# Kernel tuning notes

Hardware: AMD Instinct MI355X
Metric: run time of the kernel (lower is better)

## Reference

```python
import jax, jax.numpy as jnp
import numpy as np
from jax.scipy.linalg import solve_triangular

EPS = 1e-5
CHUNK = 64

def _rms(x, w, eps=EPS):
    return x * jax.lax.rsqrt(jnp.mean(x * x, axis=-1, keepdims=True) + eps) * w

def _l2norm(x, eps=1e-6):
    return x * jax.lax.rsqrt(jnp.sum(x * x, axis=-1, keepdims=True) + eps)

def _causal_conv(x, w):
    # x: [B,T,C], w: [C,K] depthwise causal short conv
    K = w.shape[1]
    T = x.shape[1]
    xp = jnp.pad(x, ((0, 0), (K - 1, 0), (0, 0)))
    return sum(xp[:, j:j + T, :] * w[:, j] for j in range(K))

def _chunk_gated_delta_rule(q, k, v, g, beta, chunk=CHUNK):
    # q,k: [B,H,T,Dk] (l2-normalized, q pre-scaled); v: [B,H,T,Dv]; g,beta: [B,H,T]
    Bb, H, T, Dk = k.shape
    Dv = v.shape[-1]
    N = T // chunk
    qc, kc, vc = (a.reshape(Bb, H, N, chunk, -1) for a in (q, k, v))
    gc = g.reshape(Bb, H, N, chunk)
    bc = beta.reshape(Bb, H, N, chunk)
    gcs = jnp.cumsum(gc, axis=-1)  # within-chunk cumulative log-decay
    tri = jnp.tril(jnp.ones((chunk, chunk), bool))
    tri_s = jnp.tril(jnp.ones((chunk, chunk), bool), -1)
    diff = gcs[..., :, None] - gcs[..., None, :]
    decay = jnp.where(tri, jnp.exp(jnp.where(tri, diff, 0.0)), 0.0)  # [B,H,N,C,C]
    k_beta = kc * bc[..., None]
    v_beta = vc * bc[..., None]
    A = jnp.einsum('bhnck,bhndk->bhncd', k_beta, kc) * decay
    A = jnp.where(tri_s, A, 0.0)
    eye = jnp.eye(chunk, dtype=q.dtype)
    Tmat = solve_triangular(eye + A, jnp.broadcast_to(eye, A.shape), lower=True)  # (I+A)^-1
    u = Tmat @ v_beta                               # [B,H,N,C,Dv]
    w = Tmat @ (k_beta * jnp.exp(gcs)[..., None])   # [B,H,N,C,Dk]

    def step(S, inp):
        q_i, k_i, u_i, w_i, g_i, dm_i = inp
        attn = jnp.where(tri, jnp.einsum('bhck,bhdk->bhcd', q_i, k_i) * dm_i, 0.0)
        v_new = u_i - w_i @ S
        o_i = (q_i * jnp.exp(g_i)[..., None]) @ S + attn @ v_new
        g_last = g_i[..., -1]
        k_dec = k_i * jnp.exp(g_last[..., None] - g_i)[..., None]
        S = S * jnp.exp(g_last)[..., None, None] + jnp.einsum('bhck,bhcv->bhkv', k_dec, v_new)
        return S, o_i

    xs = tuple(jnp.moveaxis(a, 2, 0) for a in (qc, kc, u, w, gcs, decay))
    S0 = jnp.zeros((Bb, H, Dk, Dv), q.dtype)
    _, outs = jax.lax.scan(step, S0, xs)  # [N,B,H,C,Dv]
    return jnp.moveaxis(outs, 0, 2).reshape(Bb, H, T, Dv)

def _layer_forward(x, mask, ln1_w, qkvz_w, ba_w, conv_w, A_log, dt_bias,
                   o_norm_w, out_w, ln2_w, gate_w, up_w, down_w):
    B, T, D = x.shape
    H = A_log.shape[0]
    kd = qkvz_w.shape[0] // 4  # key_dim == value_dim here (k_heads==v_heads, Dk==Dv)
    vd = kd
    Dk = kd // H
    Dv = vd // H
    silu = jax.nn.silu
    h = _rms(x, ln1_w)
    qkvz = h @ qkvz_w.T
    q, k, v, z = jnp.split(qkvz, [kd, 2 * kd, 2 * kd + vd], axis=-1)
    b, a = jnp.split(h @ ba_w.T, 2, axis=-1)  # [B,T,H] each
    mixed = jnp.concatenate([q, k, v], axis=-1) * mask[..., None]
    mixed = silu(_causal_conv(mixed, conv_w))
    q, k, v = jnp.split(mixed, [kd, 2 * kd], axis=-1)
    q = _l2norm(q.reshape(B, T, H, Dk))
    k = _l2norm(k.reshape(B, T, H, Dk))
    v = v.reshape(B, T, H, Dv)
    beta = jax.nn.sigmoid(b) * mask[..., None]
    g = -jnp.exp(A_log) * jax.nn.softplus(a + dt_bias) * mask[..., None]
    scale = Dk ** -0.5
    bhtd = lambda t: jnp.transpose(t, (0, 2, 1, 3))
    o = _chunk_gated_delta_rule(bhtd(q) * scale, bhtd(k), bhtd(v),
                                jnp.transpose(g, (0, 2, 1)), jnp.transpose(beta, (0, 2, 1)))
    o = jnp.transpose(o, (0, 2, 1, 3))  # [B,T,H,Dv]
    o = _rms(o, o_norm_w) * silu(z.reshape(B, T, H, Dv))  # gated RMSNorm
    x = x + o.reshape(B, T, vd) @ out_w.T
    h2 = _rms(x, ln2_w)
    mlp_out = (silu(h2 @ gate_w.T) * (h2 @ up_w.T)) @ down_w.T
    return x + mlp_out

def setup_inputs():
    key = jax.random.key(0)
    ks = jax.random.split(key, 12)
    B, T, D, H, Dk, Dv, M, K = 1, 4096, 2048, 16, 128, 128, 8192, 4
    kd, vd = H * Dk, H * Dv
    nrm = lambda i, shp, sc=0.02: jax.random.normal(ks[i], shp, jnp.float32) * sc
    return {
        'x': nrm(0, (B, T, D), 1.0),
        'mask': jnp.ones((B, T), jnp.float32),
        'ln1_w': jnp.ones((D,), jnp.float32),
        'qkvz_w': nrm(1, (2 * kd + 2 * vd, D)),
        'ba_w': nrm(2, (2 * H, D)),
        'conv_w': nrm(3, (2 * kd + vd, K), 0.3),
        'A_log': jnp.log(jax.random.uniform(ks[4], (H,), jnp.float32, 1.0, 16.0)),
        'dt_bias': nrm(5, (H,), 0.5),
        'o_norm_w': jnp.ones((Dv,), jnp.float32),
        'out_w': nrm(6, (D, vd)),
        'ln2_w': jnp.ones((D,), jnp.float32),
        'gate_w': nrm(7, (M, D)),
        'up_w': nrm(8, (M, D)),
        'down_w': nrm(9, (D, M)),
    }

def reference(x, mask, ln1_w, qkvz_w, ba_w, conv_w, A_log, dt_bias,
              o_norm_w, out_w, ln2_w, gate_w, up_w, down_w):
    return _layer_forward(x, mask, ln1_w, qkvz_w, ba_w, conv_w, A_log, dt_bias,
                          o_norm_w, out_w, ln2_w, gate_w, up_w, down_w)
```

## Files before the change

kernel.cpp:

```cpp
#include <hip/hip_runtime.h>
#include <math.h>

#define T_LEN 4096
#define DMODEL 2048
#define NH 16
#define CQKV 6144
#define CQKVZ 8192
#define SCALE 0.08838834764831845f

using bf16x8 = __attribute__((ext_vector_type(8))) short;
using f32x4  = __attribute__((ext_vector_type(4))) float;

__device__ __forceinline__ float siluf(float x) { return x / (1.0f + __expf(-x)); }

__device__ __forceinline__ unsigned short f2bf(float f) {
  unsigned int u = __float_as_uint(f);
  u = (u + 0x7FFFu + ((u >> 16) & 1u)) >> 16;
  return (unsigned short)u;
}
__device__ __forceinline__ float bf2f(unsigned short u) {
  return __uint_as_float(((unsigned int)u) << 16);
}
__device__ __forceinline__ ushort4 pack4(float a, float b, float c, float d) {
  ushort4 r; r.x = f2bf(a); r.y = f2bf(b); r.z = f2bf(c); r.w = f2bf(d); return r;
}

__device__ __forceinline__ void gl_lds16(const unsigned short* g, unsigned short* l) {
  __builtin_amdgcn_global_load_lds(
      (const __attribute__((address_space(1))) void*)g,
      (__attribute__((address_space(3))) void*)l, 16, 0, 0);
}

template<int MODE>
__global__ __launch_bounds__(256) void rmsnorm_kernel(const float* __restrict__ x,
                                                      const float* __restrict__ w,
                                                      float* __restrict__ outf,
                                                      unsigned short* __restrict__ outb) {
  const int t = blockIdx.x;
  const int tid = threadIdx.x;
  const float4* xr = (const float4*)(x + (size_t)t * DMODEL);
  float4 v0 = xr[tid];
  float4 v1 = xr[tid + 256];
  float s = v0.x*v0.x + v0.y*v0.y + v0.z*v0.z + v0.w*v0.w
          + v1.x*v1.x + v1.y*v1.y + v1.z*v1.z + v1.w*v1.w;
#pragma unroll
  for (int off = 32; off > 0; off >>= 1) s += __shfl_down(s, off);
  __shared__ float red[4];
  if ((tid & 63) == 0) red[tid >> 6] = s;
  __syncthreads();
  const float tot = red[0] + red[1] + red[2] + red[3];
  const float r = rsqrtf(tot * (1.0f / DMODEL) + 1e-5f);
  const float4* wr = (const float4*)w;
  const float4 w0 = wr[tid], w1 = wr[tid + 256];
  float4 o0, o1;
  o0.x = v0.x*r*w0.x; o0.y = v0.y*r*w0.y; o0.z = v0.z*r*w0.z; o0.w = v0.w*r*w0.w;
  o1.x = v1.x*r*w1.x; o1.y = v1.y*r*w1.y; o1.z = v1.z*r*w1.z; o1.w = v1.w*r*w1.w;
  if (MODE == 1) {
    float4* orow = (float4*)(outf + (size_t)t * DMODEL);
    orow[tid] = o0;
    orow[tid + 256] = o1;
  }
  ushort4* brow = (ushort4*)(outb + (size_t)t * DMODEL);
  brow[tid] = pack4(o0.x, o0.y, o0.z, o0.w);
  brow[tid + 256] = pack4(o1.x, o1.y, o1.z, o1.w);
}

__global__ __launch_bounds__(256) void f2b_kernel(const float* __restrict__ in,
                                                  unsigned short* __restrict__ out) {
  const size_t i = (size_t)blockIdx.x * 256 + threadIdx.x;
  const float4 a = ((const float4*)in)[2 * i];
  const float4 b = ((const float4*)in)[2 * i + 1];
  ((ushort4*)out)[2 * i] = pack4(a.x, a.y, a.z, a.w);
  ((ushort4*)out)[2 * i + 1] = pack4(b.x, b.y, b.z, b.w);
}

template<int EPI, int BM>
__global__ __launch_bounds__(512, 1) void gemm256_kernel(const unsigned short* __restrict__ A,
                                                         const unsigned short* __restrict__ B,
                                                         float* __restrict__ Cf,
                                                         unsigned short* __restrict__ Cb,
                                                         int M, int N, int K) {
  constexpr int BN = 256;
  constexpr int MI = BM / 32;
  constexpr int AW = BM / 128;
  __shared__ __align__(16) unsigned short lds[3][(BM + BN) * 32];
  const int nbm = M / BM, nbn = N / BN, nwg = nbm * nbn;
  const int nt = K >> 5;
  int bmi, bni;
  {
    const int bid = blockIdx.x;
    const int cpx = nwg >> 3;
    int sc = 1;
    while (sc * sc < cpx) sc <<= 1;
    if (sc * sc > cpx) sc >>= 1;
    const int scn = (sc > 0) ? (cpx / sc) : 0;
    if ((nwg & 7) == 0 && sc > 0 && sc * scn == cpx && (nbm % sc) == 0 && (nbn % scn) == 0) {
      const int chunk = bid & 7, widx = bid >> 3;
      const int regc = nbn / scn;
      bmi = (chunk / regc) * sc + widx / scn;
      bni = (chunk % regc) * scn + widx % scn;
    } else {
      bmi = bid / nbn; bni = bid % nbn;
    }
  }
  const int bm = bmi * BM, bn = bni * BN;
  const int tid = threadIdx.x;
  const int wv = tid >> 6, ln = tid & 63;
  const int fr = ln & 15, qq = ln >> 4;
  const int wm = wv >> 2, wn = wv & 3;
  const int ra0 = wm * (BM / 2), rb0 = wn * 64;
  const int lrow = ln >> 2;
  const int lslot = ln & 3;

  f32x4 acc[MI][4];
  const f32x4 zero = {0.f, 0.f, 0.f, 0.f};
#pragma unroll
  for (int mi = 0; mi < MI; mi++)
#pragma unroll
    for (int ni = 0; ni < 4; ni++) acc[mi][ni] = zero;

  auto stageA = [&](int buf, int t) {
    const int k0 = t << 5;
#pragma unroll
    for (int q = 0; q < AW; q++) {
      const int lr = q * 128 + wv * 16 + lrow;
      const int sl = lslot ^ ((lr >> 1) & 3);
      gl_lds16(A + (size_t)(bm + lr) * K + k0 + sl * 8,
               &lds[buf][(q * 128 + wv * 16) * 32]);
    }
  };
  auto stageB = [&](int buf, int t) {
    const int k0 = t << 5;
#pragma unroll
    for (int q = 0; q < 2; q++) {
      const int lr = q * 128 + wv * 16 + lrow;
      const int sl = lslot ^ ((lr >> 1) & 3);
      gl_lds16(B + (size_t)(bn + lr) * K + k0 + sl * 8,
               &lds[buf][BM * 32 + (q * 128 + wv * 16) * 32]);
    }
  };

  stageA(0, 0); stageB(0, 0);
  stageA(1, 1); stageB(1, 1);
  if constexpr (AW == 2) asm volatile("s_waitcnt vmcnt(4)" ::: "memory");
  else                   asm volatile("s_waitcnt vmcnt(3)" ::: "memory");
  __builtin_amdgcn_s_barrier();
  asm volatile("" ::: "memory");

  for (int t = 0; t < nt; t++) {
    const int cb = t % 3;
    const int b2 = (t + 2) % 3;
    const unsigned short* lA = &lds[cb][0];
    const unsigned short* lB = &lds[cb][BM * 32];
    bf16x8 bfr[4];
#pragma unroll
    for (int ni = 0; ni < 4; ni++) {
      const int r = rb0 + ni * 16 + fr;
      bfr[ni] = *(const bf16x8*)&lB[r * 32 + ((qq ^ ((r >> 1) & 3)) << 3)];
    }
    bf16x8 afr[MI];
#pragma unroll
    for (int mi = 0; mi < MI; mi++) {
      const int r = ra0 + mi * 16 + fr;
      afr[mi] = *(const bf16x8*)&lA[r * 32 + ((qq ^ ((r >> 1) & 3)) << 3)];
    }
    if (t + 2 < nt) { stageA(b2, t + 2); stageB(b2, t + 2); }
    __builtin_amdgcn_s_setprio(1);
#pragma unroll
    for (int mi = 0; mi < MI; mi++)
#pragma unroll
      for (int ni = 0; ni < 4; ni++)
        acc[mi][ni] = __builtin_amdgcn_mfma_f32_16x16x32_bf16(afr[mi], bfr[ni], acc[mi][ni], 0, 0, 0);
    __builtin_amdgcn_s_setprio(0);
    if (t + 1 < nt) {
      asm volatile("s_waitcnt lgkmcnt(0)" ::: "memory");
      if (t + 2 < nt) {
        if constexpr (AW == 2) asm volatile("s_waitcnt vmcnt(4)" ::: "memory");
        else                   asm volatile("s_waitcnt vmcnt(3)" ::: "memory");
      } else {
        asm volatile("s_waitcnt vmcnt(0)" ::: "memory");
      }
      __builtin_amdgcn_s_barrier();
      asm volatile("" ::: "memory");
    }
  }

  const int cm4 = qq * 4;
#pragma unroll
  for (int mi = 0; mi < MI; mi++) {
#pragma unroll
    for (int ni = 0; ni < 4; ni++) {
#pragma unroll
      for (int r = 0; r < 4; r++) {
        const int grow = bm + ra0 + mi * 16 + cm4 + r;
        const int gcol = bn + rb0 + ni * 16 + fr;
        const size_t off = (size_t)grow * N + gcol;
        const float v = acc[mi][ni][r];
        if (EPI == 0) {
          Cb[off] = f2bf(v);
        } else if (EPI == 1) {
          Cf[off] += v;
        } else {
          Cb[off] = f2bf(siluf(bf2f(Cb[off])) * v);
        }
      }
    }
  }
}

__global__ __launch_bounds__(256) void ba_gemm_kernel(const float* __restrict__ h_in,
                                                      const float* __restrict__ ba_w,
                                                      float* __restrict__ ba_out) {
  __shared__ __align__(16) float hl[2048];
  __shared__ float red[32][9];
  const int t = blockIdx.x;
  const int tid = threadIdx.x;
  const float4* hr = (const float4*)(h_in + (size_t)t * DMODEL);
  ((float4*)hl)[tid] = hr[tid];
  ((float4*)hl)[tid + 256] = hr[tid + 256];
  __syncthreads();
  const int c = tid & 31;
  const int p = tid >> 5;
  const float* wrow = ba_w + (size_t)c * DMODEL + p * 256;
  const float* hrow = hl + p * 256;
  float s = 0.f;
#pragma unroll 8
  for (int k = 0; k < 256; k++) s += hrow[k] * wrow[k];
  red[c][p] = s;
  __syncthreads();
  if (tid < 32) {
    float tot = 0.f;
#pragma unroll
    for (int q = 0; q < 8; q++) tot += red[tid][q];
    ba_out[(size_t)t * 32 + tid] = tot;
  }
}

__global__ __launch_bounds__(256) void zcopy_kernel(const unsigned short* __restrict__ qkvz,
                                                    unsigned short* __restrict__ z) {
  const int idx = blockIdx.x * 256 + threadIdx.x;
  const int t = idx >> 8;
  const int c8 = (idx & 255) * 8;
  *(uint4*)(z + (size_t)t * 2048 + c8) =
      *(const uint4*)(qkvz + (size_t)t * CQKVZ + CQKV + c8);
}

__global__ __launch_bounds__(256) void conv_silu_kernel(const unsigned short* __restrict__ qkvz,
                                                        const float* __restrict__ conv_w,
                                                        const float* __restrict__ mask,
                                                        float* __restrict__ mixed) {
  const int idx = blockIdx.x * 256 + threadIdx.x;
  const int c4 = (idx % 1536) * 4;
  const int t = idx / 1536;
  const float4 w0 = *(const float4*)(conv_w + (size_t)c4 * 4);
  const float4 w1 = *(const float4*)(conv_w + (size_t)c4 * 4 + 4);
  const float4 w2 = *(const float4*)(conv_w + (size_t)c4 * 4 + 8);
  const float4 w3 = *(const float4*)(conv_w + (size_t)c4 * 4 + 12);
  const float wj0[4] = {w0.x, w0.y, w0.z, w0.w};
  const float wj1[4] = {w1.x, w1.y, w1.z, w1.w};
  const float wj2[4] = {w2.x, w2.y, w2.z, w2.w};
  const float wj3[4] = {w3.x, w3.y, w3.z, w3.w};
  float4 acc = make_float4(0.f, 0.f, 0.f, 0.f);
#pragma unroll
  for (int j = 0; j < 4; j++) {
    const int tt = t - 3 + j;
    if (tt < 0) continue;
    const float m = mask[tt];
    const ushort4 xb = *(const ushort4*)(qkvz + (size_t)tt * CQKVZ + c4);
    acc.x += bf2f(xb.x) * m * wj0[j];
    acc.y += bf2f(xb.y) * m * wj1[j];
    acc.z += bf2f(xb.z) * m * wj2[j];
    acc.w += bf2f(xb.w) * m * wj3[j];
  }
  acc.x = siluf(acc.x); acc.y = siluf(acc.y); acc.z = siluf(acc.z); acc.w = siluf(acc.w);
  *(float4*)(mixed + (size_t)t * CQKV + c4) = acc;
}

__global__ __launch_bounds__(256) void l2norm_kernel(float* __restrict__ mixed) {
  const int r = blockIdx.x * 4 + (threadIdx.x >> 6);
  const int lane = threadIdx.x & 63;
  const int t = r >> 5;
  const int hh = r & 31;
  float* p = mixed + (size_t)t * CQKV + hh * 128 + lane * 2;
  float2 v = *(float2*)p;
  float s = v.x * v.x + v.y * v.y;
#pragma unroll
  for (int off = 32; off > 0; off >>= 1) s += __shfl_down(s, off);
  s = __shfl(s, 0);
  const float rn = rsqrtf(s + 1e-6f);
  v.x *= rn; v.y *= rn;
  *(float2*)p = v;
}

__global__ __launch_bounds__(256) void beta_g_kernel(const float* __restrict__ ba,
                                                     const float* __restrict__ A_log,
                                                     const float* __restrict__ dt_bias,
                                                     const float* __restrict__ mask,
                                                     float* __restrict__ beta,
                                                     float* __restrict__ g) {
  const int idx = blockIdx.x * 256 + threadIdx.x;
  const int t = idx >> 4;
  const int h = idx & 15;
  const float b = ba[(size_t)t * 32 + h];
  const float a = ba[(size_t)t * 32 + 16 + h];
  const float m = mask[t];
  beta[idx] = m / (1.0f + expf(-b));
  const float xx = a + dt_bias[h];
  const float sp = (xx > 20.0f) ? xx : log1pf(expf(xx));
  g[idx] = -expf(A_log[h]) * sp * m;
}

__global__ __launch_bounds__(256) void gcs_kernel(const float* __restrict__ g,
                                                  float* __restrict__ gcsbuf,
                                                  float* __restrict__ edkbuf,
                                                  float* __restrict__ egqbuf,
                                                  float* __restrict__ adecbuf) {
  const int idx = blockIdx.x * 256 + threadIdx.x;
  if (idx >= 1024) return;
  const int h = idx >> 6;
  const int n = idx & 63;
  const int t0 = n * 64;
  float s = 0.f;
  for (int i = 0; i < 64; i++) {
    s += g[(size_t)(t0 + i) * NH + h];
    gcsbuf[(size_t)idx * 64 + i] = s;
  }
  const float glast = s;
  adecbuf[idx] = __expf(glast);
  for (int i = 0; i < 64; i++) {
    const float gi = gcsbuf[(size_t)idx * 64 + i];
    edkbuf[(size_t)idx * 64 + i] = __expf(glast - gi);
    egqbuf[(size_t)idx * 64 + i] = __expf(gi) * SCALE;
  }
}

__global__ __launch_bounds__(256) void pre_attn_kernel(const float* __restrict__ mixed,
                                                       const float* __restrict__ gcsbuf,
                                                       const float* __restrict__ betabuf,
                                                       float* __restrict__ abuf,
                                                       float* __restrict__ attnbuf) {
  __shared__ __align__(16) float kl[64][132];
  __shared__ float gcs_s[64];
  __shared__ float betal[64];
  const int blk = blockIdx.x;
  const int h = blk >> 6;
  const int n = blk & 63;
  const int t0 = n * 64;
  const int tid = threadIdx.x;
  if (tid < 64) {
    gcs_s[tid] = gcsbuf[(size_t)blk * 64 + tid];
    betal[tid] = betabuf[(size_t)(t0 + tid) * NH + h];
  }
#pragma unroll
  for (int rep = 0; rep < 8; rep++) {
    const int lin = rep * 256 + tid;
    const int i = lin >> 5;
    const int d = (lin & 31) * 4;
    const float4 kv = *(const float4*)(mixed + (size_t)(t0 + i) * CQKV + 2048 + h * 128 + d);
    *(float4*)&kl[i][d] = kv;
  }
  __syncthreads();
  const int cj = tid & 15;
  const int ri = tid >> 4;
  const int i0 = ri * 4, j0 = cj * 4;
  float accA[4][4], accQ[4][4];
#pragma unroll
  for (int a = 0; a < 4; a++)
#pragma unroll
    for (int b = 0; b < 4; b++) { accA[a][b] = 0.f; accQ[a][b] = 0.f; }
  const float* qbase = mixed + (size_t)t0 * CQKV + h * 128;
#pragma unroll 4
  for (int d = 0; d < 128; d++) {
    const float kj0 = kl[j0][d], kj1 = kl[j0 + 1][d], kj2 = kl[j0 + 2][d], kj3 = kl[j0 + 3][d];
#pragma unroll
    for (int a = 0; a < 4; a++) {
      const float ka = kl[i0 + a][d];
      const float qa = qbase[(size_t)(i0 + a) * CQKV + d];
      accA[a][0] += ka * kj0; accA[a][1] += ka * kj1; accA[a][2] += ka * kj2; accA[a][3] += ka * kj3;
      accQ[a][0] += qa * kj0; accQ[a][1] += qa * kj1; accQ[a][2] += qa * kj2; accQ[a][3] += qa * kj3;
    }
  }
#pragma unroll
  for (int a = 0; a < 4; a++) {
    const int i = i0 + a;
    const float gi = gcs_s[i];
    const float bi = betal[i];
    float4 Av, Qv;
    float dec;
    dec = __expf(fminf(gi - gcs_s[j0 + 0], 0.f));
    Av.x = (i > j0 + 0) ? accA[a][0] * bi * dec : 0.f;
    Qv.x = (i >= j0 + 0) ? accQ[a][0] * dec * SCALE : 0.f;
    dec = __expf(fminf(gi - gcs_s[j0 + 1], 0.f));
    Av.y = (i > j0 + 1) ? accA[a][1] * bi * dec : 0.f;
    Qv.y = (i >= j0 + 1) ? accQ[a][1] * dec * SCALE : 0.f;
    dec = __expf(fminf(gi - gcs_s[j0 + 2], 0.f));
    Av.z = (i > j0 + 2) ? accA[a][2] * bi * dec : 0.f;
    Qv.z = (i >= j0 + 2) ? accQ[a][2] * dec * SCALE : 0.f;
    dec = __expf(fminf(gi - gcs_s[j0 + 3], 0.f));
    Av.w = (i > j0 + 3) ? accA[a][3] * bi * dec : 0.f;
    Qv.w = (i >= j0 + 3) ? accQ[a][3] * dec * SCALE : 0.f;
    *(float4*)(abuf + (size_t)blk * 4096 + i * 64 + j0) = Av;
    *(float4*)(attnbuf + (size_t)blk * 4096 + i * 64 + j0) = Qv;
  }
}

__global__ __launch_bounds__(256) void pre_solve_kernel(const float* __restrict__ abuf,
                                                        const float* __restrict__ betabuf,
                                                        float* __restrict__ tbuf) {
  __shared__ float Al[64][65];
  __shared__ float Tl[64][65];
  const int blk = blockIdx.x;
  const int h = blk >> 6;
  const int n = blk & 63;
  const int t0 = n * 64;
  const int tid = threadIdx.x;
#pragma unroll
  for (int rep = 0; rep < 4; rep++) {
    const int lin = rep * 256 + tid;
    const int i = lin >> 4;
    const int j = (lin & 15) * 4;
    const float4 av = *(const float4*)(abuf + (size_t)blk * 4096 + i * 64 + j);
    Al[i][j] = av.x; Al[i][j + 1] = av.y; Al[i][j + 2] = av.z; Al[i][j + 3] = av.w;
  }
  __syncthreads();
  if (tid < 64) {
    const int j = tid;
    const float bj = betabuf[(size_t)(t0 + j) * NH + h];
    for (int i = 0; i < 64; i++) {
      float s = (i == j) ? 1.0f : 0.0f;
      for (int l = j; l < i; l++) s -= Al[i][l] * Tl[l][j];
      Tl[i][j] = s;
    }
    for (int i = j; i < 64; i++) Tl[i][j] *= bj;
  }
  __syncthreads();
#pragma unroll
  for (int rep = 0; rep < 4; rep++) {
    const int lin = rep * 256 + tid;
    const int i = lin >> 4;
    const int j = (lin & 15) * 4;
    float4 tv;
    tv.x = Tl[i][j]; tv.y = Tl[i][j + 1]; tv.z = Tl[i][j + 2]; tv.w = Tl[i][j + 3];
    *(float4*)(tbuf + (size_t)blk * 4096 + i * 64 + j) = tv;
  }
}

__global__ __launch_bounds__(256) void pre_uw_kernel(const float* __restrict__ mixed,
                                                     const float* __restrict__ tbuf,
                                                     const float* __restrict__ gcsbuf,
                                                     float* __restrict__ ubuf,
                                                     unsigned short* __restrict__ wbf) {
  __shared__ __align__(16) float Tl[64][68];
  __shared__ __align__(16) float xl[64][132];
  __shared__ float egcs[64];
  const int blk = blockIdx.x;
  const int h = blk >> 6;
  const int n = blk & 63;
  const int t0 = n * 64;
  const int tid = threadIdx.x;
  if (tid < 64) egcs[tid] = __expf(gcsbuf[(size_t)blk * 64 + tid]);
#pragma unroll
  for (int rep = 0; rep < 4; rep++) {
    const int lin = rep * 256 + tid;
    const int i = lin >> 4;
    const int j = (lin & 15) * 4;
    const float4 tv = *(const float4*)(tbuf + (size_t)blk * 4096 + i * 64 + j);
    *(float4*)&Tl[i][j] = tv;
  }
#pragma unroll
  for (int rep = 0; rep < 8; rep++) {
    const int lin = rep * 256 + tid;
    const int i = lin >> 5;
    const int d = (lin & 31) * 4;
    const float4 vv = *(const float4*)(mixed + (size_t)(t0 + i) * CQKV + 4096 + h * 128 + d);
    *(float4*)&xl[i][d] = vv;
  }
  __syncthreads();
  const int cgu = tid & 15;
  const int riu = tid >> 4;
  const int i0 = riu * 4;
  const int d0 = cgu * 8;
  float acc[4][8];
#pragma unroll
  for (int a = 0; a < 4; a++)
#pragma unroll
    for (int b = 0; b < 8; b++) acc[a][b] = 0.f;
#pragma unroll 2
  for (int j = 0; j < 64; j++) {
    const float tv[4] = {Tl[i0][j], Tl[i0 + 1][j], Tl[i0 + 2][j], Tl[i0 + 3][j]};
    const float4 x0 = *(const float4*)&xl[j][d0];
    const float4 x1 = *(const float4*)&xl[j][d0 + 4];
    const float xv[8] = {x0.x, x0.y, x0.z, x0.w, x1.x, x1.y, x1.z, x1.w};
#pragma unroll
    for (int a = 0; a < 4; a++)
#pragma unroll
      for (int b = 0; b < 8; b++) acc[a][b] += tv[a] * xv[b];
  }
#pragma unroll
  for (int a = 0; a < 4; a++) {
    float* up = ubuf + (size_t)(t0 + i0 + a) * 2048 + h * 128 + d0;
    *(float4*)up = make_float4(acc[a][0], acc[a][1], acc[a][2], acc[a][3]);
    *(float4*)(up + 4) = make_float4(acc[a][4], acc[a][5], acc[a][6], acc[a][7]);
  }
  __syncthreads();
#pragma unroll
  for (int rep = 0; rep < 8; rep++) {
    const int lin = rep * 256 + tid;
    const int i = lin >> 5;
    const int d = (lin & 31) * 4;
    float4 kv = *(const float4*)(mixed + (size_t)(t0 + i) * CQKV + 2048 + h * 128 + d);
    const float e = egcs[i];
    kv.x *= e; kv.y *= e; kv.z *= e; kv.w *= e;
    *(float4*)&xl[i][d] = kv;
  }
  __syncthreads();
#pragma unroll
  for (int a = 0; a < 4; a++)
#pragma unroll
    for (int b = 0; b < 8; b++) acc[a][b] = 0.f;
#pragma unroll 2
  for (int j = 0; j < 64; j++) {
    const float tv[4] = {Tl[i0][j], Tl[i0 + 1][j], Tl[i0 + 2][j], Tl[i0 + 3][j]};
    const float4 x0 = *(const float4*)&xl[j][d0];
    const float4 x1 = *(const float4*)&xl[j][d0 + 4];
    const float xv[8] = {x0.x, x0.y, x0.z, x0.w, x1.x, x1.y, x1.z, x1.w};
#pragma unroll
    for (int a = 0; a < 4; a++)
#pragma unroll
      for (int b = 0; b < 8; b++) acc[a][b] += tv[a] * xv[b];
  }
#pragma unroll
  for (int a = 0; a < 4; a++) {
    const int l = i0 + a;
    unsigned short* wp = wbf + (size_t)(t0 + l) * 2048 + h * 128 + ((cgu ^ (l & 7)) << 3);
    *(ushort4*)wp = pack4(-acc[a][0], -acc[a][1], -acc[a][2], -acc[a][3]);
    *(ushort4*)(wp + 4) = pack4(-acc[a][4], -acc[a][5], -acc[a][6], -acc[a][7]);
  }
}

__global__ __launch_bounds__(256) void ktrans_kernel(const float* __restrict__ mixed,
                                                     const float* __restrict__ edkbuf,
                                                     const float* __restrict__ egqbuf,
                                                     unsigned short* __restrict__ kdT,
                                                     unsigned short* __restrict__ qe) {
  __shared__ __align__(16) float kl[64][132];
  __shared__ float edk_s[64];
  __shared__ float egq_s[64];
  const int blk = blockIdx.x;
  const int h = blk >> 6;
  const int n = blk & 63;
  const int t0 = n * 64;
  const int tid = threadIdx.x;
  if (tid < 64) {
    edk_s[tid] = edkbuf[(size_t)blk * 64 + tid];
    egq_s[tid] = egqbuf[(size_t)blk * 64 + tid];
  }
#pragma unroll
  for (int q = 0; q < 8; q++) {
    const int idx = tid + q * 256;
    const int l = idx >> 5, c4 = (idx & 31) * 4;
    *(float4*)&kl[l][c4] = *(const float4*)(mixed + (size_t)(t0 + l) * CQKV + 2048 + h * 128 + c4);
  }
  __syncthreads();
#pragma unroll
  for (int q = 0; q < 4; q++) {
    const int idx = tid + q * 256;
    const int d = idx >> 3, lsl = idx & 7;
    const int l8 = lsl * 8;
    float v[8];
#pragma unroll
    for (int j = 0; j < 8; j++) v[j] = kl[l8 + j][d] * edk_s[l8 + j];
    unsigned short* p = kdT + (size_t)blk * 8192 + d * 64 + ((lsl ^ (d & 7)) << 3);
    *(ushort4*)p = pack4(v[0], v[1], v[2], v[3]);
    *(ushort4*)(p + 4) = pack4(v[4], v[5], v[6], v[7]);
  }
#pragma unroll
  for (int q = 0; q < 8; q++) {
    const int idx = tid + q * 256;
    const int i = idx >> 5, c4 = (idx & 31) * 4;
    const float4 v = *(const float4*)(mixed + (size_t)(t0 + i) * CQKV + h * 128 + c4);
    const float e = egq_s[i];
    *(ushort4*)(qe + (size_t)(t0 + i) * 2048 + h * 128 + c4) =
        pack4(v.x * e, v.y * e, v.z * e, v.w * e);
  }
}

__global__ __launch_bounds__(512, 1) void scan_kernel(const unsigned short* __restrict__ wbf,
                                                      const unsigned short* __restrict__ kdT,
                                                      const float* __restrict__ ubuf,
                                                      const float* __restrict__ adecbuf,
                                                      unsigned short* __restrict__ STb,
                                                      unsigned short* __restrict__ vtb,
                                                      const float* __restrict__ gw,
                                                      const float* __restrict__ uw,
                                                      const float* __restrict__ dw,
                                                      const float* __restrict__ ow,
                                                      const float* __restrict__ xin,
                                                      unsigned short* __restrict__ Wg,
                                                      unsigned short* __restrict__ Wu,
                                                      unsigned short* __restrict__ Wd,
                                                      unsigned short* __restrict__ Wo,
                                                      float* __restrict__ outc) {
  __shared__ __align__(16) unsigned short stage[2][16384];
  __shared__ __align__(16) unsigned short privAll[8][3072];
  if (blockIdx.x >= 16) {
    const int xb = blockIdx.x - 16;
    const int tid = threadIdx.x;
    if (xb < 13312) {
      const float* src; unsigned short* dst; size_t u;
      if (xb < 4096)       { src = gw; dst = Wg; u = (size_t)xb * 512 + tid; }
      else if (xb < 8192)  { src = uw; dst = Wu; u = (size_t)(xb - 4096) * 512 + tid; }
      else if (xb < 12288) { src = dw; dst = Wd; u = (size_t)(xb - 8192) * 512 + tid; }
      else                 { src = ow; dst = Wo; u = (size_t)(xb - 12288) * 512 + tid; }
      const float4 a = ((const float4*)src)[2 * u];
      const float4 b = ((const float4*)src)[2 * u + 1];
      ((ushort4*)dst)[2 * u] = pack4(a.x, a.y, a.z, a.w);
      ((ushort4*)dst)[2 * u + 1] = pack4(b.x, b.y, b.z, b.w);
    } else {
      const size_t i = (size_t)(xb - 13312) * 512 + tid;
      ((float4*)outc)[2 * i] = ((const float4*)xin)[2 * i];
      ((float4*)outc)[2 * i + 1] = ((const float4*)xin)[2 * i + 1];
    }
    return;
  }
  const int h = blockIdx.x;
  const int tid = threadIdx.x;
  const int ln = tid & 63;
  const int wv = tid >> 6;
  const int fr = ln & 15;
  const int g  = ln >> 4;
  const int c0 = wv * 16;
  const int fsw = fr & 7;
  unsigned short* privA = &privAll[wv][0];
  unsigned short* privB = &privAll[wv][2048];
  const f32x4 zero = {0.f, 0.f, 0.f, 0.f};

  f32x4 acc2[8];
#pragma unroll
  for (int dt = 0; dt < 8; dt++) acc2[dt] = zero;

  auto stage_wk = [&](int buf, int n1) {
    const int t0n = n1 * 64;
    const size_t kbase = (size_t)(h * 64 + n1) * 8192;
#pragma unroll
    for (int q = 0; q < 2; q++) {
      const int m = wv * 2 + q;
      gl_lds16(wbf + (size_t)(t0n + m * 4 + (ln >> 4)) * 2048 + h * 128 + (ln & 15) * 8,
               &stage[buf][m * 512]);
      gl_lds16(kdT + kbase + (m * 8 + (ln >> 3)) * 64 + (ln & 7) * 8,
               &stage[buf][8192 + m * 512]);
    }
  };

  float ur[4][4];
#pragma unroll
  for (int lt = 0; lt < 4; lt++)
#pragma unroll
    for (int r = 0; r < 4; r++)
      ur[lt][r] = ubuf[(size_t)(lt * 16 + g * 4 + r) * 2048 + h * 128 + c0 + fr];
  float ad = adecbuf[h * 64];
  stage_wk(0, 0);
  asm volatile("s_waitcnt vmcnt(0)" ::: "memory");
  __builtin_amdgcn_s_barrier();
  asm volatile("" ::: "memory");

  for (int n = 0; n < 64; n++) {
    const int blk = h * 64 + n;
    const unsigned short* wl = &stage[n & 1][0];
    const unsigned short* kl = &stage[n & 1][8192];
    if (n + 1 < 64) stage_wk((n + 1) & 1, n + 1);
    __builtin_amdgcn_sched_barrier(0);
    float urn[4][4];
    float adn = 0.f;
    if (n + 1 < 64) {
      const int t1 = (n + 1) * 64;
#pragma unroll
      for (int lt = 0; lt < 4; lt++)
#pragma unroll
        for (int r = 0; r < 4; r++)
          urn[lt][r] = ubuf[(size_t)(t1 + lt * 16 + g * 4 + r) * 2048 + h * 128 + c0 + fr];
      adn = adecbuf[blk + 1];
    } else {
#pragma unroll
      for (int lt = 0; lt < 4; lt++)
#pragma unroll
        for (int r = 0; r < 4; r++) urn[lt][r] = 0.f;
    }
    __builtin_amdgcn_sched_barrier(0);
#pragma unroll
    for (int dt = 0; dt < 8; dt++) {
      const int slot = dt * 2 + (g >> 1);
      const ushort4 pv = pack4(acc2[dt][0], acc2[dt][1], acc2[dt][2], acc2[dt][3]);
      *(ushort4*)&privA[fr * 128 + ((slot ^ fsw) << 3) + (g & 1) * 4] = pv;
      *(ushort4*)(STb + (size_t)blk * 16384 + (c0 + fr) * 128 + dt * 16 + g * 4) = pv;
    }
    f32x4 acc1[4];
#pragma unroll
    for (int lt = 0; lt < 4; lt++) {
      f32x4 t;
      t[0] = ur[lt][0]; t[1] = ur[lt][1]; t[2] = ur[lt][2]; t[3] = ur[lt][3];
      acc1[lt] = t;
    }
#pragma unroll
    for (int ks = 0; ks < 4; ks++) {
      const int kb = ks * 4 + g;
      const bf16x8 b = *(const bf16x8*)&privA[fr * 128 + ((kb ^ fsw) << 3)];
#pragma unroll
      for (int lt = 0; lt < 4; lt++) {
        const bf16x8 a = *(const bf16x8*)&wl[(lt * 16 + fr) * 128 + ((kb ^ fsw) << 3)];
        acc1[lt] = __builtin_amdgcn_mfma_f32_16x16x32_bf16(a, b, acc1[lt], 0, 0, 0);
      }
    }
#pragma unroll
    for (int lt = 0; lt < 4; lt++) {
      const int slot = lt * 2 + (g >> 1);
      const ushort4 pv = pack4(acc1[lt][0], acc1[lt][1], acc1[lt][2], acc1[lt][3]);
      *(ushort4*)&privB[fr * 64 + ((slot ^ fsw) << 3) + (g & 1) * 4] = pv;
      *(ushort4*)(vtb + (size_t)blk * 8192 + (c0 + fr) * 64 + lt * 16 + g * 4) = pv;
    }
#pragma unroll
    for (int dt = 0; dt < 8; dt++) {
      acc2[dt][0] *= ad; acc2[dt][1] *= ad; acc2[dt][2] *= ad; acc2[dt][3] *= ad;
    }
#pragma unroll
    for (int ks = 0; ks < 2; ks++) {
      const int kb = ks * 4 + g;
      const bf16x8 b = *(const bf16x8*)&privB[fr * 64 + ((kb ^ fsw) << 3)];
#pragma unroll
      for (int dt = 0; dt < 8; dt++) {
        const bf16x8 a = *(const bf16x8*)&kl[(dt * 16 + fr) * 64 + ((kb ^ fsw) << 3)];
        acc2[dt] = __builtin_amdgcn_mfma_f32_16x16x32_bf16(a, b, acc2[dt], 0, 0, 0);
      }
    }
#pragma unroll
    for (int lt = 0; lt < 4; lt++)
#pragma unroll
      for (int r = 0; r < 4; r++) ur[lt][r] = urn[lt][r];
    ad = adn;
    if (n + 1 < 64) {
      asm volatile("s_waitcnt lgkmcnt(0)" ::: "memory");
      __builtin_amdgcn_sched_barrier(0);
      asm volatile("s_waitcnt vmcnt(29)" ::: "memory");
      __builtin_amdgcn_sched_barrier(0);
      __builtin_amdgcn_s_barrier();
      __builtin_amdgcn_sched_barrier(0);
    }
  }
}

__global__ __launch_bounds__(256) void ocomp_kernel(const unsigned short* __restrict__ qe,
                                                    const unsigned short* __restrict__ STbuf,
                                                    const unsigned short* __restrict__ vtbuf,
                                                    const float* __restrict__ attnbuf,
                                                    const unsigned short* __restrict__ zb,
                                                    const float* __restrict__ onw,
                                                    unsigned short* __restrict__ ob) {
  __shared__ __align__(16) unsigned short STl[128 * 128];
  __shared__ __align__(16) unsigned short vtl[128 * 64];
  __shared__ __align__(16) unsigned short ql[64 * 128];
  __shared__ __align__(16) unsigned short al[64 * 64];
  const int blk = blockIdx.x;
  const int h = blk >> 6;
  const int n = blk & 63;
  const int t0 = n * 64;
  const int tid = threadIdx.x;
#pragma unroll
  for (int q = 0; q < 8; q++) {
    const int idx = tid + q * 256;
    const int c = idx >> 4, dg = idx & 15;
    *(uint4*)&STl[c * 128 + ((dg ^ (c & 7)) << 3)] =
        *(const uint4*)(STbuf + (size_t)blk * 16384 + c * 128 + dg * 8);
  }
#pragma unroll
  for (int q = 0; q < 4; q++) {
    const int idx = tid + q * 256;
    const int c = idx >> 3, lg = idx & 7;
    *(uint4*)&vtl[c * 64 + ((lg ^ (c & 7)) << 3)] =
        *(const uint4*)(vtbuf + (size_t)blk * 8192 + c * 64 + lg * 8);
  }
#pragma unroll
  for (int q = 0; q < 4; q++) {
    const int idx = tid + q * 256;
    const int i = idx >> 4, dg = idx & 15;
    *(uint4*)&ql[i * 128 + ((dg ^ (i & 7)) << 3)] =
        *(const uint4*)(qe + (size_t)(t0 + i) * 2048 + h * 128 + dg * 8);
  }
#pragma unroll
  for (int q = 0; q < 4; q++) {
    const int idx = tid + q * 256;
    const int i = idx >> 4, l4 = (idx & 15) * 4;
    const float4 v = *(const float4*)(attnbuf + (size_t)blk * 4096 + i * 64 + l4);
    *(ushort4*)&al[i * 64 + (((l4 >> 3) ^ (i & 7)) << 3) + (l4 & 7)] =
        pack4(v.x, v.y, v.z, v.w);
  }
  __syncthreads();
  const int ln = tid & 63;
  const int wv = tid >> 6;
  const int fr = ln & 15;
  const int g = ln >> 4;
  const int i0 = wv * 16;
  f32x4 acc[8];
  const f32x4 zero = {0.f, 0.f, 0.f, 0.f};
#pragma unroll
  for (int nt = 0; nt < 8; nt++) acc[nt] = zero;
#pragma unroll
  for (int ks = 0; ks < 4; ks++) {
    const int kb = ks * 4 + g;
    const int ar = i0 + fr;
    const bf16x8 a = *(const bf16x8*)&ql[ar * 128 + ((kb ^ (ar & 7)) << 3)];
#pragma unroll
    for (int nt = 0; nt < 8; nt++) {
      const int c = nt * 16 + fr;
      const bf16x8 b = *(const bf16x8*)&STl[c * 128 + ((kb ^ (c & 7)) << 3)];
      acc[nt] = __builtin_amdgcn_mfma_f32_16x16x32_bf16(a, b, acc[nt], 0, 0, 0);
    }
  }
#pragma unroll
  for (int ks = 0; ks < 2; ks++) {
    const int kb = ks * 4 + g;
    const int ar = i0 + fr;
    const bf16x8 a = *(const bf16x8*)&al[ar * 64 + ((kb ^ (ar & 7)) << 3)];
#pragma unroll
    for (int nt = 0; nt < 8; nt++) {
      const int c = nt * 16 + fr;
      const bf16x8 b = *(const bf16x8*)&vtl[c * 64 + ((kb ^ (c & 7)) << 3)];
      acc[nt] = __builtin_amdgcn_mfma_f32_16x16x32_bf16(a, b, acc[nt], 0, 0, 0);
    }
  }
  float s0 = 0.f, s1 = 0.f, s2 = 0.f, s3 = 0.f;
#pragma unroll
  for (int nt = 0; nt < 8; nt++) {
    s0 += acc[nt][0] * acc[nt][0];
    s1 += acc[nt][1] * acc[nt][1];
    s2 += acc[nt][2] * acc[nt][2];
    s3 += acc[nt][3] * acc[nt][3];
  }
#pragma unroll
  for (int m = 1; m < 16; m <<= 1) {
    s0 += __shfl_xor(s0, m);
    s1 += __shfl_xor(s1, m);
    s2 += __shfl_xor(s2, m);
    s3 += __shfl_xor(s3, m);
  }
  float rn[4];
  rn[0] = rsqrtf(s0 * (1.0f / 128.0f) + 1e-5f);
  rn[1] = rsqrtf(s1 * (1.0f / 128.0f) + 1e-5f);
  rn[2] = rsqrtf(s2 * (1.0f / 128.0f) + 1e-5f);
  rn[3] = rsqrtf(s3 * (1.0f / 128.0f) + 1e-5f);
#pragma unroll
  for (int nt = 0; nt < 8; nt++) {
    const int c = nt * 16 + fr;
    const float wn = onw[c];
#pragma unroll
    for (int r = 0; r < 4; r++) {
      const size_t off = (size_t)(t0 + i0 + g * 4 + r) * 2048 + h * 128 + c;
      const float zz = siluf(bf2f(zb[off]));
      ob[off] = f2bf(acc[nt][r] * rn[r] * wn * zz);
    }
  }
}

extern "C" void kernel_launch(void* const* d_in, const int* in_sizes, int n_in,
                              void* d_out, int out_size, void* d_ws, size_t ws_size,
                              hipStream_t stream) {
  (void)in_sizes; (void)n_in; (void)out_size;
  const float* x        = (const float*)d_in[0];
  const float* mask     = (const float*)d_in[1];
  const float* ln1_w    = (const float*)d_in[2];
  const float* qkvz_w   = (const float*)d_in[3];
  const float* ba_w     = (const float*)d_in[4];
  const float* conv_w   = (const float*)d_in[5];
  const float* A_log    = (const float*)d_in[6];
  const float* dt_bias  = (const float*)d_in[7];
  const float* o_norm_w = (const float*)d_in[8];
  const float* out_w    = (const float*)d_in[9];
  const float* ln2_w    = (const float*)d_in[10];
  const float* gate_w   = (const float*)d_in[11];
  const float* up_w     = (const float*)d_in[12];
  const float* down_w   = (const float*)d_in[13];
  float* out = (float*)d_out;

  const size_t NEED_BYTES = (size_t)75825152 * 4;
  if (ws_size < NEED_BYTES) return;

  float* ws = (float*)d_ws;
  float* mixed_buf = ws;
  unsigned short* Wg = (unsigned short*)ws;
  unsigned short* Wu = (unsigned short*)(ws + 8388608);
  unsigned short* Wd = (unsigned short*)(ws + 16777216);
  unsigned short* qkvz_bf = (unsigned short*)(ws + 25165824);
  float* u_buf = ws + 25165824;
  unsigned short* wbf = (unsigned short*)(ws + 33554432);
  unsigned short* kdT = (unsigned short*)(ws + 37748736);
  unsigned short* gate_bf = (unsigned short*)(ws + 25165824);
  unsigned short* z_bf = (unsigned short*)(ws + 41943040);
  float* h_buf = ws + 46137344;
  float* a_buf = ws + 46137344;
  unsigned short* vt_buf = (unsigned short*)(ws + 46137344);
  float* t_buf = ws + 50331648;
  unsigned short* qe_bf = (unsigned short*)(ws + 50331648);
  unsigned short* h_bf  = (unsigned short*)(ws + 54525952);
  unsigned short* ob    = (unsigned short*)(ws + 54525952);
  unsigned short* h2_bf = (unsigned short*)(ws + 54525952);
  float* attn_buf = ws + 58720256;
  unsigned short* Wq = (unsigned short*)(ws + 62914560);
  unsigned short* ST_buf = (unsigned short*)(ws + 62914560);
  unsigned short* Wo = (unsigned short*)(ws + 71303168);
  float* ba_buf   = ws + 73400320;
  float* beta_buf = ws + 73531392;
  float* g_buf    = ws + 73596928;
  float* gcs_buf  = ws + 73662464;
  float* edk_buf  = ws + 73728000;
  float* egq_buf  = ws + 73793536;
  float* adec_buf = ws + 73859072;

  rmsnorm_kernel<1><<<4096, 256, 0, stream>>>(x, ln1_w, h_buf, h_bf);
  f2b_kernel<<<8192, 256, 0, stream>>>(qkvz_w, Wq);
  gemm256_kernel<0, 256><<<512, 512, 0, stream>>>(h_bf, Wq, nullptr, qkvz_bf, 4096, 8192, 2048);
  ba_gemm_kernel<<<4096, 256, 0, stream>>>(h_buf, ba_w, ba_buf);
  zcopy_kernel<<<4096, 256, 0, stream>>>(qkvz_bf, z_bf);
  conv_silu_kernel<<<24576, 256, 0, stream>>>(qkvz_bf, conv_w, mask, mixed_buf);
  l2norm_kernel<<<32768, 256, 0, stream>>>(mixed_buf);
  beta_g_kernel<<<256, 256, 0, stream>>>(ba_buf, A_log, dt_bias, mask, beta_buf, g_buf);
  gcs_kernel<<<4, 256, 0, stream>>>(g_buf, gcs_buf, edk_buf, egq_buf, adec_buf);
  pre_attn_kernel<<<1024, 256, 0, stream>>>(mixed_buf, gcs_buf, beta_buf, a_buf, attn_buf);
  pre_solve_kernel<<<1024, 256, 0, stream>>>(a_buf, beta_buf, t_buf);
  pre_uw_kernel<<<1024, 256, 0, stream>>>(mixed_buf, t_buf, gcs_buf, u_buf, wbf);
  ktrans_kernel<<<1024, 256, 0, stream>>>(mixed_buf, edk_buf, egq_buf, kdT, qe_bf);
  scan_kernel<<<15376, 512, 0, stream>>>(wbf, kdT, u_buf, adec_buf, ST_buf, vt_buf,
                                         gate_w, up_w, down_w, out_w, x,
                                         Wg, Wu, Wd, Wo, out);
  ocomp_kernel<<<1024, 256, 0, stream>>>(qe_bf, ST_buf, vt_buf, attn_buf,
                                         z_bf, o_norm_w, ob);
  gemm256_kernel<1, 128><<<256, 512, 0, stream>>>(ob, Wo, out, nullptr, 4096, 2048, 2048);
  rmsnorm_kernel<2><<<4096, 256, 0, stream>>>(out, ln2_w, nullptr, h2_bf);
  gemm256_kernel<0, 256><<<512, 512, 0, stream>>>(h2_bf, Wg, nullptr, gate_bf, 4096, 8192, 2048);
  gemm256_kernel<2, 256><<<512, 512, 0, stream>>>(h2_bf, Wu, nullptr, gate_bf, 4096, 8192, 2048);
  gemm256_kernel<1, 128><<<256, 512, 0, stream>>>(gate_bf, Wd, out, nullptr, 4096, 2048, 8192);
}
```

Before: 1.469 ms.

## Store u, state and v_new buffers in MFMA-fragment-major layout for coalesced access

Changes the intermediate buffers u, S^T and v_new to a layout grouped by MFMA fragment (rows of 4 contiguous values per column). The sequential recurrence kernel can then load u as float4 and write state/v_new with contiguous ushort4 stores instead of strided scalar accesses, and the wait count is lowered to match the fewer outstanding loads. The consumer kernel is rewritten to de-interleave the new layout into its swizzled LDS tiles. This adds more complex indexing and LDS stores of half width in the output kernel.

```diff
diff --git a/kernel.cpp b/kernel.cpp
--- a/kernel.cpp
+++ b/kernel.cpp
@@ -497,10 +497,9 @@
       for (int b = 0; b < 8; b++) acc[a][b] += tv[a] * xv[b];
   }
 #pragma unroll
-  for (int a = 0; a < 4; a++) {
-    float* up = ubuf + (size_t)(t0 + i0 + a) * 2048 + h * 128 + d0;
-    *(float4*)up = make_float4(acc[a][0], acc[a][1], acc[a][2], acc[a][3]);
-    *(float4*)(up + 4) = make_float4(acc[a][4], acc[a][5], acc[a][6], acc[a][7]);
+  for (int b = 0; b < 8; b++) {
+    *(float4*)(ubuf + (size_t)blk * 8192 + riu * 512 + (size_t)(d0 + b) * 4) =
+        make_float4(acc[0][b], acc[1][b], acc[2][b], acc[3][b]);
   }
   __syncthreads();
 #pragma unroll
@@ -652,12 +651,10 @@
     }
   };
 
-  float ur[4][4];
+  float4 ur4[4];
 #pragma unroll
   for (int lt = 0; lt < 4; lt++)
-#pragma unroll
-    for (int r = 0; r < 4; r++)
-      ur[lt][r] = ubuf[(size_t)(lt * 16 + g * 4 + r) * 2048 + h * 128 + c0 + fr];
+    ur4[lt] = *(const float4*)(ubuf + (size_t)(h * 64) * 8192 + (lt * 4 + g) * 512 + (c0 + fr) * 4);
   float ad = adecbuf[h * 64];
   stage_wk(0, 0);
   asm volatile("s_waitcnt vmcnt(0)" ::: "memory");
@@ -670,21 +667,18 @@
     const unsigned short* kl = &stage[n & 1][8192];
     if (n + 1 < 64) stage_wk((n + 1) & 1, n + 1);
     __builtin_amdgcn_sched_barrier(0);
-    float urn[4][4];
+    float4 ur4n[4];
     float adn = 0.f;
     if (n + 1 < 64) {
-      const int t1 = (n + 1) * 64;
+      const size_t ub = (size_t)(blk + 1) * 8192;
 #pragma unroll
       for (int lt = 0; lt < 4; lt++)
-#pragma unroll
-        for (int r = 0; r < 4; r++)
-          urn[lt][r] = ubuf[(size_t)(t1 + lt * 16 + g * 4 + r) * 2048 + h * 128 + c0 + fr];
+        ur4n[lt] = *(const float4*)(ubuf + ub + (lt * 4 + g) * 512 + (c0 + fr) * 4);
       adn = adecbuf[blk + 1];
     } else {
-#pragma unroll
-      for (int lt = 0; lt < 4; lt++)
-#pragma unroll
-        for (int r = 0; r < 4; r++) urn[lt][r] = 0.f;
+      const float4 z4 = make_float4(0.f, 0.f, 0.f, 0.f);
+#pragma unroll
+      for (int lt = 0; lt < 4; lt++) ur4n[lt] = z4;
     }
     __builtin_amdgcn_sched_barrier(0);
 #pragma unroll
@@ -692,13 +686,13 @@
       const int slot = dt * 2 + (g >> 1);
       const ushort4 pv = pack4(acc2[dt][0], acc2[dt][1], acc2[dt][2], acc2[dt][3]);
       *(ushort4*)&privA[fr * 128 + ((slot ^ fsw) << 3) + (g & 1) * 4] = pv;
-      *(ushort4*)(STb + (size_t)blk * 16384 + (c0 + fr) * 128 + dt * 16 + g * 4) = pv;
+      *(ushort4*)(STb + (size_t)blk * 16384 + (dt * 4 + g) * 512 + (c0 + fr) * 4) = pv;
     }
     f32x4 acc1[4];
 #pragma unroll
     for (int lt = 0; lt < 4; lt++) {
       f32x4 t;
-      t[0] = ur[lt][0]; t[1] = ur[lt][1]; t[2] = ur[lt][2]; t[3] = ur[lt][3];
+      t[0] = ur4[lt].x; t[1] = ur4[lt].y; t[2] = ur4[lt].z; t[3] = ur4[lt].w;
       acc1[lt] = t;
     }
 #pragma unroll
@@ -716,7 +710,7 @@
       const int slot = lt * 2 + (g >> 1);
       const ushort4 pv = pack4(acc1[lt][0], acc1[lt][1], acc1[lt][2], acc1[lt][3]);
       *(ushort4*)&privB[fr * 64 + ((slot ^ fsw) << 3) + (g & 1) * 4] = pv;
-      *(ushort4*)(vtb + (size_t)blk * 8192 + (c0 + fr) * 64 + lt * 16 + g * 4) = pv;
+      *(ushort4*)(vtb + (size_t)blk * 8192 + (lt * 4 + g) * 512 + (c0 + fr) * 4) = pv;
     }
 #pragma unroll
     for (int dt = 0; dt < 8; dt++) {
@@ -733,14 +727,12 @@
       }
     }
 #pragma unroll
-    for (int lt = 0; lt < 4; lt++)
-#pragma unroll
-      for (int r = 0; r < 4; r++) ur[lt][r] = urn[lt][r];
+    for (int lt = 0; lt < 4; lt++) ur4[lt] = ur4n[lt];
     ad = adn;
     if (n + 1 < 64) {
       asm volatile("s_waitcnt lgkmcnt(0)" ::: "memory");
       __builtin_amdgcn_sched_barrier(0);
-      asm volatile("s_waitcnt vmcnt(29)" ::: "memory");
+      asm volatile("s_waitcnt vmcnt(17)" ::: "memory");
       __builtin_amdgcn_sched_barrier(0);
       __builtin_amdgcn_s_barrier();
       __builtin_amdgcn_sched_barrier(0);
@@ -766,17 +758,27 @@
   const int tid = threadIdx.x;
 #pragma unroll
   for (int q = 0; q < 8; q++) {
-    const int idx = tid + q * 256;
-    const int c = idx >> 4, dg = idx & 15;
-    *(uint4*)&STl[c * 128 + ((dg ^ (c & 7)) << 3)] =
-        *(const uint4*)(STbuf + (size_t)blk * 16384 + c * 128 + dg * 8);
+    const int o = tid + q * 256;
+    const int dq = o >> 6, w = o & 63;
+    const uint4 v = *(const uint4*)(STbuf + (size_t)blk * 16384 + (size_t)o * 8);
+    const int cA = 2 * w, cB = 2 * w + 1;
+    const int base = ((dq >> 1)) ;
+    uint2 h0; h0.x = v.x; h0.y = v.y;
+    uint2 h1; h1.x = v.z; h1.y = v.w;
+    *(uint2*)&STl[cA * 128 + (((dq >> 1) ^ (cA & 7)) << 3) + (dq & 1) * 4] = h0;
+    *(uint2*)&STl[cB * 128 + (((dq >> 1) ^ (cB & 7)) << 3) + (dq & 1) * 4] = h1;
+    (void)base;
   }
 #pragma unroll
   for (int q = 0; q < 4; q++) {
-    const int idx = tid + q * 256;
-    const int c = idx >> 3, lg = idx & 7;
-    *(uint4*)&vtl[c * 64 + ((lg ^ (c & 7)) << 3)] =
-        *(const uint4*)(vtbuf + (size_t)blk * 8192 + c * 64 + lg * 8);
+    const int o = tid + q * 256;
+    const int lq = o >> 6, w = o & 63;
+    const uint4 v = *(const uint4*)(vtbuf + (size_t)blk * 8192 + (size_t)o * 8);
+    const int cA = 2 * w, cB = 2 * w + 1;
+    uint2 h0; h0.x = v.x; h0.y = v.y;
+    uint2 h1; h1.x = v.z; h1.y = v.w;
+    *(uint2*)&vtl[cA * 64 + (((lq >> 1) ^ (cA & 7)) << 3) + (lq & 1) * 4] = h0;
+    *(uint2*)&vtl[cB * 64 + (((lq >> 1) ^ (cB & 7)) << 3) + (lq & 1) * 4] = h1;
   }
 #pragma unroll
   for (int q = 0; q < 4; q++) {
```

Measured after the change: 1.372 ms. -6.6%, faster.
